# Optimization experiments

Measured on AMD Instinct MI355X. Metric: run time of the kernel, lower is better.

## Reference

```python
import jax, jax.numpy as jnp
import numpy as np

T, H = 2048, 1024
NH, NKV, HD = 8, 2, 128
E, TOPK, NG, TKG = 16, 4, 4, 2
F, FS = 1024, 1024
EPS = 1e-6
ROUTED_SCALE = 2.0
THETA = 10000.0


def _rmsnorm(x, w):
    return x * jax.lax.rsqrt(jnp.mean(x * x, axis=-1, keepdims=True) + EPS) * w


def setup_inputs() -> dict:
    key = jax.random.key(0)
    ks = jax.random.split(key, 12)
    s = 0.02
    return {
        "hidden_states": jax.random.normal(ks[0], (T, H), jnp.float32),
        "residual": jax.random.normal(ks[1], (T, H), jnp.float32),
        "position_ids": jnp.arange(T, dtype=jnp.int32),
        "ln1_w": jnp.ones((H,), jnp.float32),
        "qkv_w": s * jax.random.normal(ks[2], (H, (NH + 2 * NKV) * HD), jnp.float32),
        "qnorm_w": jnp.ones((HD,), jnp.float32),
        "knorm_w": jnp.ones((HD,), jnp.float32),
        "dense_w": s * jax.random.normal(ks[3], (NH * HD, H), jnp.float32),
        "ln2_w": jnp.ones((H,), jnp.float32),
        "gate_w": s * jax.random.normal(ks[4], (H, E), jnp.float32),
        "expert_bias": 0.1 * jax.random.normal(ks[5], (E,), jnp.float32),
        "w13": s * jax.random.normal(ks[6], (E, H, 2 * F), jnp.float32),
        "w2": s * jax.random.normal(ks[7], (E, F, H), jnp.float32),
        "ws_gate_up": s * jax.random.normal(ks[8], (H, 2 * FS), jnp.float32),
        "ws_down": s * jax.random.normal(ks[9], (FS, H), jnp.float32),
    }


def block_forward(hidden_states, residual, position_ids, ln1_w, qkv_w, qnorm_w,
                  knorm_w, dense_w, ln2_w, gate_w, expert_bias, w13, w2,
                  ws_gate_up, ws_down):
    # fused add + RMSNorm (input_layernorm with residual)
    resid = hidden_states + residual
    h = _rmsnorm(resid, ln1_w)

    # --- attention ---
    qkv = h @ qkv_w  # [T, (NH+2*NKV)*HD]
    q = qkv[:, : NH * HD].reshape(T, NH, HD)
    k = qkv[:, NH * HD : (NH + NKV) * HD].reshape(T, NKV, HD)
    v = qkv[:, (NH + NKV) * HD :].reshape(T, NKV, HD)
    q = _rmsnorm(q, qnorm_w)  # qk-norm per head_dim
    k = _rmsnorm(k, knorm_w)

    # neox-style RoPE over full head_dim
    inv_freq = 1.0 / (THETA ** (jnp.arange(0, HD, 2, dtype=jnp.float32) / HD))
    ang = position_ids.astype(jnp.float32)[:, None] * inv_freq[None, :]  # [T, HD/2]
    cos = jnp.cos(ang)[:, None, :]
    sin = jnp.sin(ang)[:, None, :]

    def rope(x):
        x1, x2 = x[..., : HD // 2], x[..., HD // 2 :]
        return jnp.concatenate([x1 * cos - x2 * sin, x2 * cos + x1 * sin], axis=-1)

    q, k = rope(q), rope(k)
    rep = NH // NKV
    kr = jnp.repeat(k, rep, axis=1)  # [T, NH, HD]
    vr = jnp.repeat(v, rep, axis=1)

    scores = jnp.einsum("qhd,khd->hqk", q, kr) * (HD ** -0.5)
    causal = jnp.tril(jnp.ones((T, T), bool))
    scores = jnp.where(causal[None], scores, jnp.finfo(scores.dtype).min)
    probs = jax.nn.softmax(scores, axis=-1)
    ctx = jnp.einsum("hqk,khd->qhd", probs, vr).reshape(T, NH * HD)
    attn_out = ctx @ dense_w

    # fused add + RMSNorm (post_attention_layernorm)
    resid2 = attn_out + resid
    h2 = _rmsnorm(resid2, ln2_w)

    # --- MoE router: sigmoid scoring + correction bias, grouped top-k ---
    logits = h2.astype(jnp.float32) @ gate_w  # router in fp32
    s_scores = jax.nn.sigmoid(logits)  # [T, E]
    sfc = s_scores + expert_bias[None, :]
    gview = sfc.reshape(T, NG, E // NG)
    gscores = jax.lax.top_k(gview, 2)[0].sum(-1)  # sum of top-2 per group
    gidx = jax.lax.top_k(gscores, TKG)[1]  # [T, TKG]
    gmask = jax.nn.one_hot(gidx, NG, dtype=sfc.dtype).sum(1)  # [T, NG]
    smask = jnp.repeat(gmask, E // NG, axis=1)  # [T, E]
    masked = jnp.where(smask > 0, sfc, -jnp.inf)
    topk_idx = jax.lax.top_k(masked, TOPK)[1]  # [T, TOPK]
    topk_w = jnp.take_along_axis(s_scores, topk_idx, axis=1)  # weights w/o bias
    topk_w = topk_w / (topk_w.sum(-1, keepdims=True) + 1e-20)  # renormalize
    combine = (jax.nn.one_hot(topk_idx, E, dtype=topk_w.dtype) * topk_w[..., None]).sum(1)  # [T, E]

    # routed experts (dense-over-experts reference for the grouped GEMM)
    gu = jnp.einsum("th,ehf->tef", h2, w13)  # [T, E, 2F]
    g, u = gu[..., :F], gu[..., F:]
    act = jax.nn.silu(g) * u
    y = jnp.einsum("tef,efh->teh", act, w2)
    routed = jnp.einsum("teh,te->th", y, combine) * ROUTED_SCALE

    # shared expert (SwiGLU MLP)
    su = h2 @ ws_gate_up
    shared = (jax.nn.silu(su[:, :FS]) * su[:, FS:]) @ ws_down

    mlp_out = routed + shared
    return mlp_out, resid2


def reference(hidden_states, residual, position_ids, ln1_w, qkv_w, qnorm_w,
              knorm_w, dense_w, ln2_w, gate_w, expert_bias, w13, w2,
              ws_gate_up, ws_down):
    return block_forward(hidden_states, residual, position_ids, ln1_w, qkv_w,
                         qnorm_w, knorm_w, dense_w, ln2_w, gate_w, expert_bias,
                         w13, w2, ws_gate_up, ws_down)
```

## Files before the change

kernel.cpp:

```cpp
#include <hip/hip_runtime.h>
#include <hip/hip_bf16.h>


#define T_TOK 2048
#define H_DIM 1024
#define NHEAD 8
#define NKVH 2
#define HDIM 128
#define QKV_DIM 1536
#define E_EXP 16
#define TOPKE 4
#define F_DIM 1024
#define FS_DIM 1024
#define NPAIR (T_TOK*TOPKE)
#define EPS_F 1e-6f

#define DEV __device__ __forceinline__

typedef __attribute__((ext_vector_type(4))) float f32x4;
typedef __attribute__((ext_vector_type(8))) short s16x8;

DEV float us2f(unsigned short u){ return __uint_as_float(((unsigned int)u)<<16); }
DEV unsigned short f2us(float f){
  __hip_bfloat16 b = __float2bfloat16(f);
  unsigned short u; __builtin_memcpy(&u,&b,2); return u;
}

DEV void gl2lds16(const void* g, void* l){
  __builtin_amdgcn_global_load_lds(
      (const __attribute__((address_space(1))) void*)g,
      (__attribute__((address_space(3))) void*)l, 16, 0, 0);
}

DEV int crow(int qt){ int a=qt>>2, b=qt&3; return (a+1)*(2*a+b); }

DEV float bred_sum(float v, float* sm){
  #pragma unroll
  for(int o=32;o>0;o>>=1) v += __shfl_down(v,o);
  int w = threadIdx.x>>6, l = threadIdx.x&63;
  __syncthreads();
  if(l==0) sm[w]=v;
  __syncthreads();
  return sm[0]+sm[1]+sm[2]+sm[3];
}

__global__ __launch_bounds__(256) void k_cvt_t(const float* __restrict__ in,
    unsigned short* __restrict__ out, int Kd, int Nd){
  const int z = blockIdx.z;
  const int kb = blockIdx.y*32, nb = blockIdx.x*32;
  __shared__ float Lt[32][33];
  const int tid = threadIdx.x;
  const int r = tid>>3, c4 = (tid&7)*4;
  const float* src = in + (long long)z*Kd*Nd + (long long)(kb+r)*Nd + nb + c4;
  float4 v = *(const float4*)src;
  Lt[r][c4+0]=v.x; Lt[r][c4+1]=v.y; Lt[r][c4+2]=v.z; Lt[r][c4+3]=v.w;
  __syncthreads();
  ushort4 o;
  o.x = f2us(Lt[c4+0][r]); o.y = f2us(Lt[c4+1][r]);
  o.z = f2us(Lt[c4+2][r]); o.w = f2us(Lt[c4+3][r]);
  *(ushort4*)(out + (long long)z*Nd*Kd + (long long)(nb+r)*Kd + kb + c4) = o;
}

__global__ __launch_bounds__(256) void k_cvt_t3(const float* __restrict__ in,
    unsigned short* __restrict__ oh, unsigned short* __restrict__ ol,
    int Kd, int Nd){
  const int kb = blockIdx.y*32, nb = blockIdx.x*32;
  __shared__ float Lt[32][33];
  const int tid = threadIdx.x;
  const int r = tid>>3, c4 = (tid&7)*4;
  const float* src = in + (long long)(kb+r)*Nd + nb + c4;
  float4 v = *(const float4*)src;
  Lt[r][c4+0]=v.x; Lt[r][c4+1]=v.y; Lt[r][c4+2]=v.z; Lt[r][c4+3]=v.w;
  __syncthreads();
  ushort4 h4, l4;
  float f;
  f = Lt[c4+0][r]; h4.x = f2us(f); l4.x = f2us(f - us2f(h4.x));
  f = Lt[c4+1][r]; h4.y = f2us(f); l4.y = f2us(f - us2f(h4.y));
  f = Lt[c4+2][r]; h4.z = f2us(f); l4.z = f2us(f - us2f(h4.z));
  f = Lt[c4+3][r]; h4.w = f2us(f); l4.w = f2us(f - us2f(h4.w));
  const long long ob = (long long)(nb+r)*Kd + kb + c4;
  *(ushort4*)(oh + ob) = h4;
  *(ushort4*)(ol + ob) = l4;
}

template<bool GROUPED, bool GATHER>
__global__ __launch_bounds__(256) void gemm_mfma(
    const unsigned short* __restrict__ A, int lda,
    const unsigned short* __restrict__ Bt, int ldbt, long long bstride,
    unsigned short* __restrict__ C, int ldc,
    const int* __restrict__ rowidx, const int* __restrict__ grpoff,
    int Mdense, int K){
  const int z = blockIdx.z;
  const int rb = GROUPED ? grpoff[z] : 0;
  const int re = GROUPED ? grpoff[z+1] : Mdense;
  const int m0 = rb + blockIdx.y*128;
  if(m0 >= re) return;
  const int n0 = blockIdx.x*128;
  const unsigned short* Bz = Bt + (long long)z*bstride;

  __shared__ unsigned short As[128][32];
  __shared__ unsigned short Bs[128][32];

  const int tid = threadIdx.x;
  const int s0 = tid, s1 = tid+256;
  int gr0 = m0 + (s0>>2), gr1 = m0 + (s1>>2);
  if(GROUPED){ gr0 = min(gr0, re-1); gr1 = min(gr1, re-1); }
  if(GATHER){ gr0 = rowidx[gr0]; gr1 = rowidx[gr1]; }
  const unsigned short* ag0 = A + (long long)gr0*lda + (s0&3)*8;
  const unsigned short* ag1 = A + (long long)gr1*lda + (s1&3)*8;
  const unsigned short* bg0 = Bz + (long long)(n0 + (s0>>2))*ldbt + (s0&3)*8;
  const unsigned short* bg1 = Bz + (long long)(n0 + (s1>>2))*ldbt + (s1&3)*8;
  char* asb = (char*)&As[0][0];
  char* bsb = (char*)&Bs[0][0];
  const int wb = (tid & 192)*16;

  const int w = tid>>6, lane = tid&63;
  const int wm = (w>>1)*64, wn = (w&1)*64;
  const int fr = lane&15, q8 = (lane>>4)*8;

  f32x4 zero = {0.f,0.f,0.f,0.f};
  f32x4 acc[4][4];
  #pragma unroll
  for(int mi=0;mi<4;mi++)
    #pragma unroll
    for(int ni=0;ni<4;ni++) acc[mi][ni]=zero;

  for(int k0=0;k0<K;k0+=32){
    __syncthreads();
    gl2lds16(ag0 + k0, asb + wb);
    gl2lds16(ag1 + k0, asb + 4096 + wb);
    gl2lds16(bg0 + k0, bsb + wb);
    gl2lds16(bg1 + k0, bsb + 4096 + wb);
    __syncthreads();
    s16x8 af[4], bf[4];
    #pragma unroll
    for(int mi=0;mi<4;mi++) af[mi] = *(const s16x8*)&As[wm+mi*16+fr][q8];
    #pragma unroll
    for(int ni=0;ni<4;ni++) bf[ni] = *(const s16x8*)&Bs[wn+ni*16+fr][q8];
    #pragma unroll
    for(int mi=0;mi<4;mi++)
      #pragma unroll
      for(int ni=0;ni<4;ni++)
        acc[mi][ni] = __builtin_amdgcn_mfma_f32_16x16x32_bf16(af[mi], bf[ni], acc[mi][ni], 0,0,0);
  }
  const int q4 = (lane>>4)*4;
  #pragma unroll
  for(int mi=0;mi<4;mi++)
    #pragma unroll
    for(int ni=0;ni<4;ni++){
      const int col = n0 + wn + ni*16 + fr;
      #pragma unroll
      for(int r=0;r<4;r++){
        const int row = m0 + wm + mi*16 + q4 + r;
        if(row < re) C[(long long)row*ldc + col] = f2us(acc[mi][ni][r]);
      }
    }
}

template<int EPI_ADD>
__global__ __launch_bounds__(256) void gemm_mfma3(
    const unsigned short* __restrict__ Ah, const unsigned short* __restrict__ Al, int lda,
    const unsigned short* __restrict__ Bh, const unsigned short* __restrict__ Bl, int ldbt,
    float* __restrict__ C, int ldc, const float* __restrict__ D, int K){
  const int m0 = blockIdx.y*128;
  const int n0 = blockIdx.x*128;

  __shared__ unsigned short Ash[128][32];
  __shared__ unsigned short Asl[128][32];
  __shared__ unsigned short Bsh[128][32];
  __shared__ unsigned short Bsl[128][32];

  const int tid = threadIdx.x;
  const int s0 = tid, s1 = tid+256;
  const long long ar0 = (long long)(m0 + (s0>>2))*lda + (s0&3)*8;
  const long long ar1 = (long long)(m0 + (s1>>2))*lda + (s1&3)*8;
  const long long br0 = (long long)(n0 + (s0>>2))*ldbt + (s0&3)*8;
  const long long br1 = (long long)(n0 + (s1>>2))*ldbt + (s1&3)*8;
  char* ahb = (char*)&Ash[0][0];
  char* alb = (char*)&Asl[0][0];
  char* bhb = (char*)&Bsh[0][0];
  char* blb = (char*)&Bsl[0][0];
  const int wb = (tid & 192)*16;

  const int w = tid>>6, lane = tid&63;
  const int wm = (w>>1)*64, wn = (w&1)*64;
  const int fr = lane&15, q8 = (lane>>4)*8;

  f32x4 zero = {0.f,0.f,0.f,0.f};
  f32x4 acc[4][4];
  #pragma unroll
  for(int mi=0;mi<4;mi++)
    #pragma unroll
    for(int ni=0;ni<4;ni++) acc[mi][ni]=zero;

  for(int k0=0;k0<K;k0+=32){
    __syncthreads();
    gl2lds16(Ah + ar0 + k0, ahb + wb);
    gl2lds16(Ah + ar1 + k0, ahb + 4096 + wb);
    gl2lds16(Al + ar0 + k0, alb + wb);
    gl2lds16(Al + ar1 + k0, alb + 4096 + wb);
    gl2lds16(Bh + br0 + k0, bhb + wb);
    gl2lds16(Bh + br1 + k0, bhb + 4096 + wb);
    gl2lds16(Bl + br0 + k0, blb + wb);
    gl2lds16(Bl + br1 + k0, blb + 4096 + wb);
    __syncthreads();
    s16x8 afh[4], afl[4], bfh[4], bfl[4];
    #pragma unroll
    for(int mi=0;mi<4;mi++){
      afh[mi] = *(const s16x8*)&Ash[wm+mi*16+fr][q8];
      afl[mi] = *(const s16x8*)&Asl[wm+mi*16+fr][q8];
    }
    #pragma unroll
    for(int ni=0;ni<4;ni++){
      bfh[ni] = *(const s16x8*)&Bsh[wn+ni*16+fr][q8];
      bfl[ni] = *(const s16x8*)&Bsl[wn+ni*16+fr][q8];
    }
    #pragma unroll
    for(int mi=0;mi<4;mi++)
      #pragma unroll
      for(int ni=0;ni<4;ni++){
        acc[mi][ni] = __builtin_amdgcn_mfma_f32_16x16x32_bf16(afh[mi], bfh[ni], acc[mi][ni], 0,0,0);
        acc[mi][ni] = __builtin_amdgcn_mfma_f32_16x16x32_bf16(afh[mi], bfl[ni], acc[mi][ni], 0,0,0);
        acc[mi][ni] = __builtin_amdgcn_mfma_f32_16x16x32_bf16(afl[mi], bfh[ni], acc[mi][ni], 0,0,0);
      }
  }
  const int q4 = (lane>>4)*4;
  #pragma unroll
  for(int mi=0;mi<4;mi++)
    #pragma unroll
    for(int ni=0;ni<4;ni++){
      const int col = n0 + wn + ni*16 + fr;
      #pragma unroll
      for(int r=0;r<4;r++){
        const int row = m0 + wm + mi*16 + q4 + r;
        float v = acc[mi][ni][r];
        if(EPI_ADD) v += D[(long long)row*ldc + col];
        C[(long long)row*ldc + col] = v;
      }
    }
}

__global__ __launch_bounds__(256) void k_silu(const unsigned short* __restrict__ gu,
    unsigned short* __restrict__ act){
  const int r = blockIdx.x, c = threadIdx.x*4;
  const ushort4 g4 = *(const ushort4*)(gu + (long long)r*2048 + c);
  const ushort4 u4 = *(const ushort4*)(gu + (long long)r*2048 + 1024 + c);
  float g[4] = {us2f(g4.x),us2f(g4.y),us2f(g4.z),us2f(g4.w)};
  float u[4] = {us2f(u4.x),us2f(u4.y),us2f(u4.z),us2f(u4.w)};
  ushort4 o;
  o.x = f2us((g[0]/(1.f+__expf(-g[0])))*u[0]);
  o.y = f2us((g[1]/(1.f+__expf(-g[1])))*u[1]);
  o.z = f2us((g[2]/(1.f+__expf(-g[2])))*u[2]);
  o.w = f2us((g[3]/(1.f+__expf(-g[3])))*u[3]);
  *(ushort4*)(act + (long long)r*1024 + c) = o;
}

__global__ __launch_bounds__(256) void k_add_rmsnorm(const float* __restrict__ hs,
    const float* __restrict__ rs, const float* __restrict__ w,
    float* __restrict__ resid, unsigned short* __restrict__ ah,
    unsigned short* __restrict__ al){
  int t = blockIdx.x, tid = threadIdx.x;
  __shared__ float sm[4];
  const long base = (long)t*H_DIM;
  float x[4]; float ss = 0.f;
  #pragma unroll
  for(int i=0;i<4;i++){
    int c = tid + i*256;
    float v = hs[base+c] + rs[base+c];
    x[i]=v; resid[base+c]=v; ss += v*v;
  }
  float tot = bred_sum(ss, sm);
  float rms = rsqrtf(tot/(float)H_DIM + EPS_F);
  #pragma unroll
  for(int i=0;i<4;i++){
    int c = tid + i*256;
    float v = x[i]*rms*w[c];
    unsigned short hh = f2us(v);
    ah[base+c] = hh;
    al[base+c] = f2us(v - us2f(hh));
  }
}

__global__ __launch_bounds__(64) void k_qkv_post(const float* __restrict__ qkv,
    const float* __restrict__ qw, const float* __restrict__ kw,
    const int* __restrict__ pos,
    float* __restrict__ qb, float* __restrict__ kb, float* __restrict__ vb){
  int slot = blockIdx.x, t = blockIdx.y, lane = threadIdx.x;
  const float* x = qkv + (long long)t*QKV_DIM + slot*HDIM;
  float x0 = x[lane], x1 = x[lane+64];
  if(slot < 10){
    float ss = x0*x0 + x1*x1;
    #pragma unroll
    for(int o=32;o>0;o>>=1) ss += __shfl_xor(ss,o);
    float rms = rsqrtf(ss/(float)HDIM + EPS_F);
    const float* w = (slot<8)? qw : kw;
    float n0 = x0*rms*w[lane];
    float n1 = x1*rms*w[lane+64];
    float p = (float)pos[t];
    float invf = __expf(-((float)lane/64.f)*9.210340371976184f);
    float ang = p*invf;
    float s = sinf(ang), c = cosf(ang);
    float o0 = n0*c - n1*s;
    float o1 = n1*c + n0*s;
    float* dst = (slot<8)? (qb + ((long long)slot*T_TOK + t)*HDIM)
                         : (kb + ((long long)(slot-8)*T_TOK + t)*HDIM);
    dst[lane]=o0; dst[lane+64]=o1;
  } else {
    float* dst = vb + ((long long)(slot-10)*T_TOK + t)*HDIM;
    dst[lane]=x0; dst[lane+64]=x1;
  }
}

#define FBQ 32
#define FBK 128
__global__ __launch_bounds__(256,2) void k_flash(const float* __restrict__ qb,
    const float* __restrict__ kb, const float* __restrict__ vb,
    float* __restrict__ ctx, float* __restrict__ Op1, float* __restrict__ Op2,
    float* __restrict__ Ml){
  const int b = blockIdx.x;
  const int u0 = (17*b)>>1, u1 = (17*(b+1))>>1;
  const int tid = threadIdx.x;
  const int lane = tid & 63;
  const int w = tid >> 6;
  const int tx = tid & 31;
  const int ty = tid >> 5;
  const int fsw = tx & 7;

  __shared__ float4 smem4[4096];
  char*  smem = (char*)smem4;
  float* Ksf  = (float*)smem;
  float* Psf  = (float*)(smem + 49152);

  const float scale = 0.08838834764831845f;

  int h = u0/544;
  int r = u0 - h*544;
  int qt = 0;
  while(qt < 63 && crow(qt+1) <= r) qt++;
  int kt = r - crow(qt);

  int u = u0;
  while(u < u1){
    const int nkt = (qt>>2) + 1;
    const int q0 = qt * FBQ;
    const int kv = h >> 2;
    const float* kbase = kb + (long long)kv*T_TOK*HDIM;
    const float* vbase = vb + (long long)kv*T_TOK*HDIM;
    const float* qrow0 = qb + ((long long)h*T_TOK + q0 + ty*4)*HDIM;
    const int segN = min(nkt - kt, u1 - u);
    const int ktEnd = kt + segN;

    float m_[4], l_[4], O[4][4];
    #pragma unroll
    for(int qi=0;qi<4;qi++){
      m_[qi] = -1e30f; l_[qi] = 0.f;
      #pragma unroll
      for(int j=0;j<4;j++) O[qi][j] = 0.f;
    }

    for(; kt<ktEnd; kt++){
      const int k0 = kt * FBK;
      __syncthreads();
      {
        const float* kcur = kbase + (long long)k0*HDIM;
        #pragma unroll
        for(int i=0;i<16;i++){
          const int rbase = (w<<5) + (i<<1);
          const int f = (i>>1) & 7;
          const float* src = kcur + (long long)(rbase + (lane>>5))*HDIM
                                  + (((lane&31)^f)<<2);
          gl2lds16(src, smem + rbase*512);
        }
      }
      __syncthreads();

      float s[4][4];
      #pragma unroll
      for(int qi=0;qi<4;qi++)
        #pragma unroll
        for(int ki=0;ki<4;ki++) s[qi][ki] = 0.f;

      #pragma unroll 2
      for(int dc=0; dc<32; dc++){
        float4 qv[4];
        #pragma unroll
        for(int qi=0;qi<4;qi++) qv[qi] = *(const float4*)(qrow0 + qi*HDIM + dc*4);
        float4 kf[4];
        #pragma unroll
        for(int ki=0;ki<4;ki++)
          kf[ki] = *(const float4*)&Ksf[(size_t)(4*tx+ki)*128 + ((dc ^ fsw)<<2)];
        #pragma unroll
        for(int qi=0;qi<4;qi++)
          #pragma unroll
          for(int ki=0;ki<4;ki++){
            s[qi][ki] = fmaf(qv[qi].x, kf[ki].x, s[qi][ki]);
            s[qi][ki] = fmaf(qv[qi].y, kf[ki].y, s[qi][ki]);
            s[qi][ki] = fmaf(qv[qi].z, kf[ki].z, s[qi][ki]);
            s[qi][ki] = fmaf(qv[qi].w, kf[ki].w, s[qi][ki]);
          }
      }

      const bool last = (kt == nkt-1);
      float rm[4];
      #pragma unroll
      for(int qi=0;qi<4;qi++){
        #pragma unroll
        for(int ki=0;ki<4;ki++){
          float v = s[qi][ki]*scale;
          if(last && (k0 + 4*tx + ki > q0 + ty*4 + qi)) v = -1e30f;
          s[qi][ki] = v;
        }
        rm[qi] = fmaxf(fmaxf(s[qi][0],s[qi][1]), fmaxf(s[qi][2],s[qi][3]));
      }
      #pragma unroll
      for(int o=1;o<32;o<<=1){
        #pragma unroll
        for(int qi=0;qi<4;qi++) rm[qi] = fmaxf(rm[qi], __shfl_xor(rm[qi], o));
      }
      float a_[4], rs[4];
      #pragma unroll
      for(int qi=0;qi<4;qi++){
        float mn = fmaxf(m_[qi], rm[qi]);
        a_[qi] = __expf(m_[qi] - mn);
        m_[qi] = mn;
        float rr = 0.f;
        #pragma unroll
        for(int ki=0;ki<4;ki++){ s[qi][ki] = __expf(s[qi][ki] - mn); rr += s[qi][ki]; }
        rs[qi] = rr;
      }
      #pragma unroll
      for(int o=1;o<32;o<<=1){
        #pragma unroll
        for(int qi=0;qi<4;qi++) rs[qi] += __shfl_xor(rs[qi], o);
      }
      #pragma unroll
      for(int qi=0;qi<4;qi++){
        l_[qi] = l_[qi]*a_[qi] + rs[qi];
        #pragma unroll
        for(int j=0;j<4;j++) O[qi][j] *= a_[qi];
      }

      __syncthreads();
      #pragma unroll
      for(int ki=0;ki<4;ki++){
        float4 pv;
        pv.x = s[0][ki]; pv.y = s[1][ki]; pv.z = s[2][ki]; pv.w = s[3][ki];
        *(float4*)&Psf[(size_t)(4*tx+ki)*32 + ((ty ^ fsw)<<2)] = pv;
      }
      __syncthreads();

      const float* vcur = vbase + (long long)k0*HDIM + tx*4;
      #pragma unroll 4
      for(int k=0;k<FBK;k++){
        float4 p4 = *(const float4*)&Psf[(size_t)k*32 + ((ty ^ ((k>>2)&7))<<2)];
        float4 vv = *(const float4*)(vcur + (size_t)k*HDIM);
        O[0][0]=fmaf(p4.x,vv.x,O[0][0]); O[0][1]=fmaf(p4.x,vv.y,O[0][1]);
        O[0][2]=fmaf(p4.x,vv.z,O[0][2]); O[0][3]=fmaf(p4.x,vv.w,O[0][3]);
        O[1][0]=fmaf(p4.y,vv.x,O[1][0]); O[1][1]=fmaf(p4.y,vv.y,O[1][1]);
        O[1][2]=fmaf(p4.y,vv.z,O[1][2]); O[1][3]=fmaf(p4.y,vv.w,O[1][3]);
        O[2][0]=fmaf(p4.z,vv.x,O[2][0]); O[2][1]=fmaf(p4.z,vv.y,O[2][1]);
        O[2][2]=fmaf(p4.z,vv.z,O[2][2]); O[2][3]=fmaf(p4.z,vv.w,O[2][3]);
        O[3][0]=fmaf(p4.w,vv.x,O[3][0]); O[3][1]=fmaf(p4.w,vv.y,O[3][1]);
        O[3][2]=fmaf(p4.w,vv.z,O[3][2]); O[3][3]=fmaf(p4.w,vv.w,O[3][3]);
      }
    }

    {
      const int R = (h<<6) + qt;
      const int S = h*544 + crow(qt);
      const int bS = (2*S+1)/17;
      const int j = b - bS;
      #pragma unroll
      for(int qi=0;qi<4;qi++){
        const int row = ty*4 + qi;
        float4 o4 = make_float4(O[qi][0],O[qi][1],O[qi][2],O[qi][3]);
        if(j==0){
          *(float4*)(ctx + (long long)(q0+row)*(NHEAD*HDIM) + h*HDIM + tx*4) = o4;
        } else if(j==1){
          *(float4*)(Op1 + (long long)R*4096 + row*128 + tx*4) = o4;
        } else {
          *(float4*)(Op2 + (long long)R*4096 + row*128 + tx*4) = o4;
        }
        if(tx==0){
          Ml[((R*3+j)<<6) + row*2 + 0] = m_[qi];
          Ml[((R*3+j)<<6) + row*2 + 1] = l_[qi];
        }
      }
    }

    u += segN;
    if(ktEnd == nkt){ kt = 0; qt++; if(qt == 64){ qt = 0; h++; } }
    else kt = ktEnd;
  }
}

__global__ __launch_bounds__(256) void k_fmerge(const float* __restrict__ ctx,
    const float* __restrict__ Op1, const float* __restrict__ Op2,
    const float* __restrict__ Ml, unsigned short* __restrict__ ch,
    unsigned short* __restrict__ cl){
  const int wv = threadIdx.x>>6, lane = threadIdx.x&63;
  const int gr = blockIdx.x*4 + wv;
  const int R = gr>>5, q = gr&31;
  const int h = R>>6, qt = R&63;
  const int nkt = (qt>>2)+1;
  const int S = h*544 + crow(qt);
  const int bS = (2*S+1)/17;
  const int bE = (2*(S+nkt-1)+1)/17;
  const int parts = bE - bS + 1;
  const float* src0 = ctx + (long long)(qt*32+q)*(NHEAD*HDIM) + h*HDIM + lane*2;
  float2 o0 = *(const float2*)src0;
  const float* mlb = Ml + ((R*3)<<6) + q*2;
  const float m0 = mlb[0], l0 = mlb[1];
  float ox, oy;
  if(parts == 1){
    float inv = 1.f/l0;
    ox = o0.x*inv; oy = o0.y*inv;
  } else {
    const float m1 = mlb[64], l1 = mlb[65];
    float2 o1 = *(const float2*)(Op1 + (long long)R*4096 + q*128 + lane*2);
    if(parts == 2){
      float mx = fmaxf(m0,m1);
      float a0 = __expf(m0-mx), a1 = __expf(m1-mx);
      float inv = 1.f/(l0*a0 + l1*a1);
      ox = (o0.x*a0 + o1.x*a1)*inv;
      oy = (o0.y*a0 + o1.y*a1)*inv;
    } else {
      const float m2 = mlb[128], l2 = mlb[129];
      float2 o2 = *(const float2*)(Op2 + (long long)R*4096 + q*128 + lane*2);
      float mx = fmaxf(fmaxf(m0,m1),m2);
      float a0 = __expf(m0-mx), a1 = __expf(m1-mx), a2 = __expf(m2-mx);
      float inv = 1.f/(l0*a0 + l1*a1 + l2*a2);
      ox = (o0.x*a0 + o1.x*a1 + o2.x*a2)*inv;
      oy = (o0.y*a0 + o1.y*a1 + o2.y*a2)*inv;
    }
  }
  const long long idx = (long long)(qt*32+q)*(NHEAD*HDIM) + h*HDIM + lane*2;
  unsigned short hx = f2us(ox), hy = f2us(oy);
  ch[idx] = hx;   cl[idx] = f2us(ox - us2f(hx));
  ch[idx+1] = hy; cl[idx+1] = f2us(oy - us2f(hy));
}

__global__ __launch_bounds__(256) void k_rms2(const float* __restrict__ r2,
    const float* __restrict__ w, float* __restrict__ h2f,
    unsigned short* __restrict__ h2b){
  int t = blockIdx.x, tid = threadIdx.x;
  __shared__ float sm[4];
  const long base = (long)t*H_DIM;
  float x[4]; float ss=0.f;
  #pragma unroll
  for(int i=0;i<4;i++){
    int c = tid+i*256;
    float v = r2[base+c];
    x[i]=v; ss += v*v;
  }
  float tot = bred_sum(ss, sm);
  float rms = rsqrtf(tot/(float)H_DIM + EPS_F);
  #pragma unroll
  for(int i=0;i<4;i++){
    int c = tid+i*256;
    float v = x[i]*rms*w[c];
    h2f[base+c] = v;
    h2b[base+c] = f2us(v);
  }
}

__global__ __launch_bounds__(256) void k_router(const float* __restrict__ h2,
    const float* __restrict__ gw, const float* __restrict__ eb,
    int* __restrict__ topk_idx, float* __restrict__ topk_w, int* __restrict__ counts){
  int t = blockIdx.x, tid = threadIdx.x;
  int e = tid & 15, seg = tid >> 4;
  const float* hrow = h2 + (long long)t*H_DIM;
  float part = 0.f;
  #pragma unroll 4
  for(int i=0;i<64;i++){
    int hh = seg*64 + i;
    part += hrow[hh]*gw[hh*E_EXP + e];
  }
  __shared__ float pm[16][17];
  __shared__ float sS[16], sfc[16];
  pm[seg][e] = part;
  __syncthreads();
  if(tid < 16){
    float l = 0.f;
    #pragma unroll
    for(int s=0;s<16;s++) l += pm[s][tid];
    float sg = 1.f/(1.f+expf(-l));
    sS[tid]=sg; sfc[tid]=sg+eb[tid];
  }
  __syncthreads();
  if(tid==0){
    float gs[4];
    #pragma unroll
    for(int g=0; g<4; g++){
      float m1=-1e30f, m2=-1e30f;
      for(int j=0;j<4;j++){
        float v=sfc[g*4+j];
        if(v>m1){ m2=m1; m1=v; } else if(v>m2){ m2=v; }
      }
      gs[g]=m1+m2;
    }
    int g1=0; for(int g=1;g<4;g++) if(gs[g]>gs[g1]) g1=g;
    int g2=-1; for(int g=0;g<4;g++){ if(g==g1) continue; if(g2<0||gs[g]>gs[g2]) g2=g; }
    bool taken[16];
    #pragma unroll
    for(int i=0;i<16;i++) taken[i]=false;
    int idx[4];
    for(int j=0;j<4;j++){
      int best=-1; float bv=-1e30f;
      for(int i=0;i<16;i++){
        int g=i>>2;
        if(g!=g1 && g!=g2) continue;
        if(taken[i]) continue;
        if(best<0 || sfc[i]>bv){ best=i; bv=sfc[i]; }
      }
      taken[best]=true; idx[j]=best;
    }
    float w[4]; float s=0.f;
    #pragma unroll
    for(int j=0;j<4;j++){ w[j]=sS[idx[j]]; s+=w[j]; }
    s += 1e-20f;
    #pragma unroll
    for(int j=0;j<4;j++){
      topk_idx[t*4+j]=idx[j];
      topk_w[t*4+j]=w[j]/s;
      atomicAdd(&counts[idx[j]],1);
    }
  }
}

__global__ void k_zero(int* __restrict__ counts){ if(threadIdx.x<16) counts[threadIdx.x]=0; }

__global__ void k_scan(const int* __restrict__ counts, int* __restrict__ offs, int* __restrict__ cursor){
  if(threadIdx.x==0){
    int s=0;
    for(int e2=0;e2<16;e2++){ offs[e2]=s; cursor[e2]=s; s+=counts[e2]; }
    offs[16]=s;
  }
}

__global__ __launch_bounds__(256) void k_scatter(const int* __restrict__ topk_idx,
    int* __restrict__ cursor, int* __restrict__ pair_tok, int* __restrict__ tok2pair){
  int i = blockIdx.x*256 + threadIdx.x;
  int e = topk_idx[i];
  int pos = atomicAdd(&cursor[e],1);
  pair_tok[pos] = i>>2;
  tok2pair[i] = pos;
}

__global__ __launch_bounds__(256) void k_combine(const unsigned short* __restrict__ y,
    const unsigned short* __restrict__ sout, const int* __restrict__ tok2pair,
    const float* __restrict__ topk_w, float* __restrict__ out0){
  int t = blockIdx.x, tid = threadIdx.x;
  int p[4]; float w[4];
  #pragma unroll
  for(int j=0;j<4;j++){ p[j]=tok2pair[t*4+j]; w[j]=topk_w[t*4+j]*2.0f; }
  const long base = (long)t*H_DIM;
  #pragma unroll
  for(int i=0;i<4;i++){
    int c = tid + i*256;
    float v = us2f(sout[base+c]);
    #pragma unroll
    for(int j=0;j<4;j++) v += w[j]*us2f(y[(long long)p[j]*H_DIM + c]);
    out0[base+c] = v;
  }
}

extern "C" void kernel_launch(void* const* d_in, const int* in_sizes, int n_in,
                              void* d_out, int out_size, void* d_ws, size_t ws_size,
                              hipStream_t stream) {
  const float* hs   = (const float*)d_in[0];
  const float* rsd  = (const float*)d_in[1];
  const int*   pos  = (const int*)d_in[2];
  const float* ln1  = (const float*)d_in[3];
  const float* qkvw = (const float*)d_in[4];
  const float* qnw  = (const float*)d_in[5];
  const float* knw  = (const float*)d_in[6];
  const float* dw   = (const float*)d_in[7];
  const float* ln2  = (const float*)d_in[8];
  const float* gw   = (const float*)d_in[9];
  const float* eb   = (const float*)d_in[10];
  const float* w13  = (const float*)d_in[11];
  const float* w2   = (const float*)d_in[12];
  const float* wsgu = (const float*)d_in[13];
  const float* wsd  = (const float*)d_in[14];
  float* out0 = (float*)d_out;
  float* out1 = out0 + (size_t)T_TOK*H_DIM;

  char* W = (char*)d_ws;
  float* resid = (float*)(W + 0);
  unsigned short* ah = (unsigned short*)(W + 8388608);
  unsigned short* al = (unsigned short*)(W + 12582912);
  float* ctx   = (float*)(W + 8388608);
  float* qkv   = (float*)(W + 16777216);
  float* qb    = (float*)(W + 29360128);
  float* h2f   = (float*)(W + 37748736);
  float* kb    = (float*)(W + 46137344);
  float* vb    = (float*)(W + 48234496);
  float* Op1   = (float*)(W + 16777216);
  float* Ml    = (float*)(W + 25165824);
  float* Op2   = (float*)(W + 37748736);
  unsigned short* cth = (unsigned short*)(W + 29360128);
  unsigned short* ctl = (unsigned short*)(W + 33554432);
  unsigned short* qwt_h = (unsigned short*)(W + 37748736);
  unsigned short* qwt_l = (unsigned short*)(W + 40894464);
  unsigned short* dwt_h = (unsigned short*)(W + 50331648);
  unsigned short* dwt_l = (unsigned short*)(W + 52428800);
  unsigned short* gu    = (unsigned short*)(W + 8388608);
  unsigned short* ybuf  = (unsigned short*)(W + 8388608);
  unsigned short* sgu   = (unsigned short*)(W + 16777216);
  unsigned short* sact  = (unsigned short*)(W + 0);
  unsigned short* sout  = (unsigned short*)(W + 46137344);
  unsigned short* h2b   = (unsigned short*)(W + 50331648);
  unsigned short* act   = (unsigned short*)(W + 54525952);
  unsigned short* w13t  = (unsigned short*)(W + 71303168);
  unsigned short* w2t   = (unsigned short*)(W + 138412032);
  unsigned short* wsgut = (unsigned short*)(W + 171966464);
  unsigned short* wsdt  = (unsigned short*)(W + 176160768);
  float* topkw = (float*)(W + 178257920);
  int* topki   = (int*)(W + 178290688);
  int* ptok    = (int*)(W + 178323456);
  int* t2p     = (int*)(W + 178356224);
  int* cnt     = (int*)(W + 178388992);
  int* offs    = (int*)(W + 178389056);
  int* cur     = (int*)(W + 178389184);

  k_cvt_t<<<dim3(64,32,16), 256, 0, stream>>>(w13,  w13t,  1024, 2048);
  k_cvt_t<<<dim3(32,32,16), 256, 0, stream>>>(w2,   w2t,   1024, 1024);
  k_cvt_t<<<dim3(64,32,1),  256, 0, stream>>>(wsgu, wsgut, 1024, 2048);
  k_cvt_t<<<dim3(32,32,1),  256, 0, stream>>>(wsd,  wsdt,  1024, 1024);
  k_cvt_t3<<<dim3(48,32,1), 256, 0, stream>>>(qkvw, qwt_h, qwt_l, 1024, 1536);
  k_cvt_t3<<<dim3(32,32,1), 256, 0, stream>>>(dw,   dwt_h, dwt_l, 1024, 1024);
  k_add_rmsnorm<<<T_TOK, 256, 0, stream>>>(hs, rsd, ln1, resid, ah, al);
  gemm_mfma3<0><<<dim3(QKV_DIM/128, T_TOK/128), 256, 0, stream>>>(
      ah, al, 1024, qwt_h, qwt_l, 1024, qkv, QKV_DIM, nullptr, 1024);
  k_qkv_post<<<dim3(12, T_TOK), 64, 0, stream>>>(qkv, qnw, knw, pos, qb, kb, vb);
  k_flash<<<512, 256, 0, stream>>>(qb, kb, vb, ctx, Op1, Op2, Ml);
  k_fmerge<<<4096, 256, 0, stream>>>(ctx, Op1, Op2, Ml, cth, ctl);
  gemm_mfma3<1><<<dim3(H_DIM/128, T_TOK/128), 256, 0, stream>>>(
      cth, ctl, 1024, dwt_h, dwt_l, 1024, out1, H_DIM, resid, 1024);
  k_rms2<<<T_TOK, 256, 0, stream>>>(out1, ln2, h2f, h2b);
  k_zero<<<1, 64, 0, stream>>>(cnt);
  k_router<<<T_TOK, 256, 0, stream>>>(h2f, gw, eb, topki, topkw, cnt);
  k_scan<<<1, 64, 0, stream>>>(cnt, offs, cur);
  k_scatter<<<NPAIR/256, 256, 0, stream>>>(topki, cur, ptok, t2p);
  gemm_mfma<false,false><<<dim3(16,16,1), 256, 0, stream>>>(
      h2b, 1024, wsgut, 1024, 0, sgu, 2048, nullptr, nullptr, T_TOK, 1024);
  k_silu<<<T_TOK, 256, 0, stream>>>(sgu, sact);
  gemm_mfma<false,false><<<dim3(8,16,1), 256, 0, stream>>>(
      sact, 1024, wsdt, 1024, 0, sout, 1024, nullptr, nullptr, T_TOK, 1024);
  gemm_mfma<true,true><<<dim3(16,64,16), 256, 0, stream>>>(
      h2b, 1024, w13t, 1024, (long long)2048*1024, gu, 2048, ptok, offs, 0, 1024);
  k_silu<<<NPAIR, 256, 0, stream>>>(gu, act);
  gemm_mfma<true,false><<<dim3(8,64,16), 256, 0, stream>>>(
      act, 1024, w2t, 1024, (long long)1024*1024, ybuf, 1024, nullptr, offs, 0, 1024);
  k_combine<<<T_TOK, 256, 0, stream>>>(ybuf, sout, t2p, topkw, out0);
}
```

Baseline: 935.8 us.

## Compute flash attention QK^T with split-bf16 MFMA and rebalance work over 768 blocks

```diff
diff --git a/kernel.cpp b/kernel.cpp
--- a/kernel.cpp
+++ b/kernel.cpp
@@ -284,7 +284,9 @@
 __global__ __launch_bounds__(64) void k_qkv_post(const float* __restrict__ qkv,
     const float* __restrict__ qw, const float* __restrict__ kw,
     const int* __restrict__ pos,
-    float* __restrict__ qb, float* __restrict__ kb, float* __restrict__ vb){
+    unsigned short* __restrict__ qbh, unsigned short* __restrict__ qbl,
+    unsigned short* __restrict__ kbh, unsigned short* __restrict__ kbl,
+    float* __restrict__ vb){
   int slot = blockIdx.x, t = blockIdx.y, lane = threadIdx.x;
   const float* x = qkv + (long long)t*QKV_DIM + slot*HDIM;
   float x0 = x[lane], x1 = x[lane+64];
@@ -302,9 +304,14 @@
     float s = sinf(ang), c = cosf(ang);
     float o0 = n0*c - n1*s;
     float o1 = n1*c + n0*s;
-    float* dst = (slot<8)? (qb + ((long long)slot*T_TOK + t)*HDIM)
-                         : (kb + ((long long)(slot-8)*T_TOK + t)*HDIM);
-    dst[lane]=o0; dst[lane+64]=o1;
+    long long base = (slot<8)? ((long long)slot*T_TOK + t)*HDIM
+                             : ((long long)(slot-8)*T_TOK + t)*HDIM;
+    unsigned short* dh = (slot<8)? qbh : kbh;
+    unsigned short* dl = (slot<8)? qbl : kbl;
+    unsigned short h0 = f2us(o0);
+    dh[base+lane] = h0;        dl[base+lane] = f2us(o0 - us2f(h0));
+    unsigned short h1 = f2us(o1);
+    dh[base+lane+64] = h1;     dl[base+lane+64] = f2us(o1 - us2f(h1));
   } else {
     float* dst = vb + ((long long)(slot-10)*T_TOK + t)*HDIM;
     dst[lane]=x0; dst[lane+64]=x1;
@@ -313,40 +320,46 @@
 
 #define FBQ 32
 #define FBK 128
-__global__ __launch_bounds__(256,2) void k_flash(const float* __restrict__ qb,
-    const float* __restrict__ kb, const float* __restrict__ vb,
-    float* __restrict__ ctx, float* __restrict__ Op1, float* __restrict__ Op2,
+__global__ __launch_bounds__(256,3) void k_flash(
+    const unsigned short* __restrict__ qbh, const unsigned short* __restrict__ qbl,
+    const unsigned short* __restrict__ kbh, const unsigned short* __restrict__ kbl,
+    const float* __restrict__ vb, float* __restrict__ ctx,
+    float* __restrict__ Op1, float* __restrict__ Op2, float* __restrict__ Op3,
     float* __restrict__ Ml){
   const int b = blockIdx.x;
-  const int u0 = (17*b)>>1, u1 = (17*(b+1))>>1;
+  const int u0 = (17*b)/3, u1 = (17*(b+1))/3;
   const int tid = threadIdx.x;
   const int lane = tid & 63;
   const int w = tid >> 6;
   const int tx = tid & 31;
   const int ty = tid >> 5;
-  const int fsw = tx & 7;
-
-  __shared__ float4 smem4[4096];
-  char*  smem = (char*)smem4;
-  float* Ksf  = (float*)smem;
-  float* Psf  = (float*)(smem + 49152);
+  const int fr = lane & 15;
+  const int l4 = lane >> 4;
+
+  __shared__ float4 ps4[1024];
+  __shared__ float Ms[4][32];
+  __shared__ float Ls[4][32];
+  __shared__ float Mn[32];
+  float* Psf = (float*)ps4;
 
   const float scale = 0.08838834764831845f;
 
   int h = u0/544;
-  int r = u0 - h*544;
+  int r0 = u0 - h*544;
   int qt = 0;
-  while(qt < 63 && crow(qt+1) <= r) qt++;
-  int kt = r - crow(qt);
+  while(qt < 63 && crow(qt+1) <= r0) qt++;
+  int kt = r0 - crow(qt);
 
   int u = u0;
   while(u < u1){
     const int nkt = (qt>>2) + 1;
     const int q0 = qt * FBQ;
     const int kv = h >> 2;
-    const float* kbase = kb + (long long)kv*T_TOK*HDIM;
+    const unsigned short* qhp = qbh + ((long long)h*T_TOK + q0)*HDIM;
+    const unsigned short* qlp = qbl + ((long long)h*T_TOK + q0)*HDIM;
+    const unsigned short* khb = kbh + (long long)kv*T_TOK*HDIM;
+    const unsigned short* klb = kbl + (long long)kv*T_TOK*HDIM;
     const float* vbase = vb + (long long)kv*T_TOK*HDIM;
-    const float* qrow0 = qb + ((long long)h*T_TOK + q0 + ty*4)*HDIM;
     const int segN = min(nkt - kt, u1 - u);
     const int ktEnd = kt + segN;
 
@@ -360,95 +373,132 @@
 
     for(; kt<ktEnd; kt++){
       const int k0 = kt * FBK;
+      f32x4 sa[2][2];
+      f32x4 zero = {0.f,0.f,0.f,0.f};
+      sa[0][0]=zero; sa[0][1]=zero; sa[1][0]=zero; sa[1][1]=zero;
+      const unsigned short* khp = khb + (long long)(k0 + w*32)*HDIM;
+      const unsigned short* klp = klb + (long long)(k0 + w*32)*HDIM;
+      #pragma unroll
+      for(int dw=0; dw<4; dw++){
+        const int doff = dw*32 + l4*8;
+        s16x8 a0h = *(const s16x8*)(qhp + (long long)fr*HDIM + doff);
+        s16x8 a0l = *(const s16x8*)(qlp + (long long)fr*HDIM + doff);
+        s16x8 a1h = *(const s16x8*)(qhp + (long long)(16+fr)*HDIM + doff);
+        s16x8 a1l = *(const s16x8*)(qlp + (long long)(16+fr)*HDIM + doff);
+        s16x8 b0h = *(const s16x8*)(khp + (long long)fr*HDIM + doff);
+        s16x8 b0l = *(const s16x8*)(klp + (long long)fr*HDIM + doff);
+        s16x8 b1h = *(const s16x8*)(khp + (long long)(16+fr)*HDIM + doff);
+        s16x8 b1l = *(const s16x8*)(klp + (long long)(16+fr)*HDIM + doff);
+        sa[0][0] = __builtin_amdgcn_mfma_f32_16x16x32_bf16(a0h,b0h,sa[0][0],0,0,0);
+        sa[0][0] = __builtin_amdgcn_mfma_f32_16x16x32_bf16(a0h,b0l,sa[0][0],0,0,0);
+        sa[0][0] = __builtin_amdgcn_mfma_f32_16x16x32_bf16(a0l,b0h,sa[0][0],0,0,0);
+        sa[0][1] = __builtin_amdgcn_mfma_f32_16x16x32_bf16(a0h,b1h,sa[0][1],0,0,0);
+        sa[0][1] = __builtin_amdgcn_mfma_f32_16x16x32_bf16(a0h,b1l,sa[0][1],0,0,0);
+        sa[0][1] = __builtin_amdgcn_mfma_f32_16x16x32_bf16(a0l,b1h,sa[0][1],0,0,0);
+        sa[1][0] = __builtin_amdgcn_mfma_f32_16x16x32_bf16(a1h,b0h,sa[1][0],0,0,0);
+        sa[1][0] = __builtin_amdgcn_mfma_f32_16x16x32_bf16(a1h,b0l,sa[1][0],0,0,0);
+        sa[1][0] = __builtin_amdgcn_mfma_f32_16x16x32_bf16(a1l,b0h,sa[1][0],0,0,0);
+        sa[1][1] = __builtin_amdgcn_mfma_f32_16x16x32_bf16(a1h,b1h,sa[1][1],0,0,0);
+        sa[1][1] = __builtin_amdgcn_mfma_f32_16x16x32_bf16(a1h,b1l,sa[1][1],0,0,0);
+        sa[1][1] = __builtin_amdgcn_mfma_f32_16x16x32_bf16(a1l,b1h,sa[1][1],0,0,0);
+      }
+
+      const bool last = (kt == nkt-1);
+      const int kg0 = k0 + w*32 + fr;
+      const int kg1 = kg0 + 16;
+      float rm[2][4];
+      #pragma unroll
+      for(int q2=0;q2<2;q2++){
+        #pragma unroll
+        for(int r=0;r<4;r++){
+          const int qg = q0 + q2*16 + l4*4 + r;
+          float v0 = sa[q2][0][r]*scale;
+          float v1 = sa[q2][1][r]*scale;
+          if(last && kg0 > qg) v0 = -1e30f;
+          if(last && kg1 > qg) v1 = -1e30f;
+          sa[q2][0][r] = v0; sa[q2][1][r] = v1;
+          rm[q2][r] = fmaxf(v0, v1);
+        }
+      }
+      #pragma unroll
+      for(int o=1;o<16;o<<=1){
+        #pragma unroll
+        for(int q2=0;q2<2;q2++)
+          #pragma unroll
+          for(int r=0;r<4;r++)
+            rm[q2][r] = fmaxf(rm[q2][r], __shfl_xor(rm[q2][r], o));
+      }
+      if(fr==0){
+        #pragma unroll
+        for(int q2=0;q2<2;q2++)
+          #pragma unroll
+          for(int r=0;r<4;r++)
+            Ms[w][q2*16 + l4*4 + r] = rm[q2][r];
+      }
       __syncthreads();
-      {
-        const float* kcur = kbase + (long long)k0*HDIM;
-        #pragma unroll
-        for(int i=0;i<16;i++){
-          const int rbase = (w<<5) + (i<<1);
-          const int f = (i>>1) & 7;
-          const float* src = kcur + (long long)(rbase + (lane>>5))*HDIM
-                                  + (((lane&31)^f)<<2);
-          gl2lds16(src, smem + rbase*512);
+
+      #pragma unroll
+      for(int qi=0;qi<4;qi++){
+        const int row = ty*4 + qi;
+        float g = fmaxf(fmaxf(Ms[0][row],Ms[1][row]), fmaxf(Ms[2][row],Ms[3][row]));
+        float mn = fmaxf(m_[qi], g);
+        float a = __expf(m_[qi] - mn);
+        m_[qi] = mn;
+        l_[qi] *= a;
+        #pragma unroll
+        for(int j=0;j<4;j++) O[qi][j] *= a;
+      }
+      if(tx==0){
+        #pragma unroll
+        for(int qi=0;qi<4;qi++) Mn[ty*4+qi] = m_[qi];
+      }
+      __syncthreads();
+
+      float rsum[2][4];
+      #pragma unroll
+      for(int q2=0;q2<2;q2++)
+        #pragma unroll
+        for(int r=0;r<4;r++) rsum[q2][r] = 0.f;
+      #pragma unroll
+      for(int q2=0;q2<2;q2++){
+        float mnv[4];
+        #pragma unroll
+        for(int r=0;r<4;r++) mnv[r] = Mn[q2*16 + l4*4 + r];
+        #pragma unroll
+        for(int k2=0;k2<2;k2++){
+          const int kl = w*32 + k2*16 + fr;
+          const int qc = q2*4 + l4;
+          float4 pv;
+          float p;
+          p = __expf(sa[q2][k2][0] - mnv[0]); pv.x = p; rsum[q2][0] += p;
+          p = __expf(sa[q2][k2][1] - mnv[1]); pv.y = p; rsum[q2][1] += p;
+          p = __expf(sa[q2][k2][2] - mnv[2]); pv.z = p; rsum[q2][2] += p;
+          p = __expf(sa[q2][k2][3] - mnv[3]); pv.w = p; rsum[q2][3] += p;
+          *(float4*)&Psf[(size_t)kl*32 + ((qc ^ ((kl>>2)&7))<<2)] = pv;
         }
       }
+      #pragma unroll
+      for(int o=1;o<16;o<<=1){
+        #pragma unroll
+        for(int q2=0;q2<2;q2++)
+          #pragma unroll
+          for(int r=0;r<4;r++)
+            rsum[q2][r] += __shfl_xor(rsum[q2][r], o);
+      }
+      if(fr==0){
+        #pragma unroll
+        for(int q2=0;q2<2;q2++)
+          #pragma unroll
+          for(int r=0;r<4;r++)
+            Ls[w][q2*16 + l4*4 + r] = rsum[q2][r];
+      }
       __syncthreads();
 
-      float s[4][4];
-      #pragma unroll
-      for(int qi=0;qi<4;qi++)
-        #pragma unroll
-        for(int ki=0;ki<4;ki++) s[qi][ki] = 0.f;
-
-      #pragma unroll 2
-      for(int dc=0; dc<32; dc++){
-        float4 qv[4];
-        #pragma unroll
-        for(int qi=0;qi<4;qi++) qv[qi] = *(const float4*)(qrow0 + qi*HDIM + dc*4);
-        float4 kf[4];
-        #pragma unroll
-        for(int ki=0;ki<4;ki++)
-          kf[ki] = *(const float4*)&Ksf[(size_t)(4*tx+ki)*128 + ((dc ^ fsw)<<2)];
-        #pragma unroll
-        for(int qi=0;qi<4;qi++)
-          #pragma unroll
-          for(int ki=0;ki<4;ki++){
-            s[qi][ki] = fmaf(qv[qi].x, kf[ki].x, s[qi][ki]);
-            s[qi][ki] = fmaf(qv[qi].y, kf[ki].y, s[qi][ki]);
-            s[qi][ki] = fmaf(qv[qi].z, kf[ki].z, s[qi][ki]);
-            s[qi][ki] = fmaf(qv[qi].w, kf[ki].w, s[qi][ki]);
-          }
-      }
-
-      const bool last = (kt == nkt-1);
-      float rm[4];
       #pragma unroll
       for(int qi=0;qi<4;qi++){
-        #pragma unroll
-        for(int ki=0;ki<4;ki++){
-          float v = s[qi][ki]*scale;
-          if(last && (k0 + 4*tx + ki > q0 + ty*4 + qi)) v = -1e30f;
-          s[qi][ki] = v;
-        }
-        rm[qi] = fmaxf(fmaxf(s[qi][0],s[qi][1]), fmaxf(s[qi][2],s[qi][3]));
-      }
-      #pragma unroll
-      for(int o=1;o<32;o<<=1){
-        #pragma unroll
-        for(int qi=0;qi<4;qi++) rm[qi] = fmaxf(rm[qi], __shfl_xor(rm[qi], o));
-      }
-      float a_[4], rs[4];
-      #pragma unroll
-      for(int qi=0;qi<4;qi++){
-        float mn = fmaxf(m_[qi], rm[qi]);
-        a_[qi] = __expf(m_[qi] - mn);
-        m_[qi] = mn;
-        float rr = 0.f;
-        #pragma unroll
-        for(int ki=0;ki<4;ki++){ s[qi][ki] = __expf(s[qi][ki] - mn); rr += s[qi][ki]; }
-        rs[qi] = rr;
-      }
-      #pragma unroll
-      for(int o=1;o<32;o<<=1){
-        #pragma unroll
-        for(int qi=0;qi<4;qi++) rs[qi] += __shfl_xor(rs[qi], o);
-      }
-      #pragma unroll
-      for(int qi=0;qi<4;qi++){
-        l_[qi] = l_[qi]*a_[qi] + rs[qi];
-        #pragma unroll
-        for(int j=0;j<4;j++) O[qi][j] *= a_[qi];
-      }
-
-      __syncthreads();
-      #pragma unroll
-      for(int ki=0;ki<4;ki++){
-        float4 pv;
-        pv.x = s[0][ki]; pv.y = s[1][ki]; pv.z = s[2][ki]; pv.w = s[3][ki];
-        *(float4*)&Psf[(size_t)(4*tx+ki)*32 + ((ty ^ fsw)<<2)] = pv;
-      }
-      __syncthreads();
-
+        const int row = ty*4 + qi;
+        l_[qi] += Ls[0][row] + Ls[1][row] + Ls[2][row] + Ls[3][row];
+      }
       const float* vcur = vbase + (long long)k0*HDIM + tx*4;
       #pragma unroll 4
       for(int k=0;k<FBK;k++){
@@ -468,7 +518,7 @@
     {
       const int R = (h<<6) + qt;
       const int S = h*544 + crow(qt);
-      const int bS = (2*S+1)/17;
+      const int bS = (3*S+2)/17;
       const int j = b - bS;
       #pragma unroll
       for(int qi=0;qi<4;qi++){
@@ -478,12 +528,14 @@
           *(float4*)(ctx + (long long)(q0+row)*(NHEAD*HDIM) + h*HDIM + tx*4) = o4;
         } else if(j==1){
           *(float4*)(Op1 + (long long)R*4096 + row*128 + tx*4) = o4;
+        } else if(j==2){
+          *(float4*)(Op2 + (long long)R*4096 + row*128 + tx*4) = o4;
         } else {
-          *(float4*)(Op2 + (long long)R*4096 + row*128 + tx*4) = o4;
+          *(float4*)(Op3 + (long long)R*4096 + row*128 + tx*4) = o4;
         }
         if(tx==0){
-          Ml[((R*3+j)<<6) + row*2 + 0] = m_[qi];
-          Ml[((R*3+j)<<6) + row*2 + 1] = l_[qi];
+          Ml[((R*4+j)<<6) + row*2 + 0] = m_[qi];
+          Ml[((R*4+j)<<6) + row*2 + 1] = l_[qi];
         }
       }
     }
@@ -496,48 +548,40 @@
 
 __global__ __launch_bounds__(256) void k_fmerge(const float* __restrict__ ctx,
     const float* __restrict__ Op1, const float* __restrict__ Op2,
-    const float* __restrict__ Ml, unsigned short* __restrict__ ch,
-    unsigned short* __restrict__ cl){
-  const int wv = threadIdx.x>>6, lane = threadIdx.x&63;
+    const float* __restrict__ Op3, const float* __restrict__ Ml,
+    unsigned short* __restrict__ ch, unsigned short* __restrict__ cl){
+  const int wv = threadIdx.x>>6, ln = threadIdx.x&63;
   const int gr = blockIdx.x*4 + wv;
   const int R = gr>>5, q = gr&31;
   const int h = R>>6, qt = R&63;
   const int nkt = (qt>>2)+1;
   const int S = h*544 + crow(qt);
-  const int bS = (2*S+1)/17;
-  const int bE = (2*(S+nkt-1)+1)/17;
+  const int bS = (3*S+2)/17;
+  const int bE = (3*(S+nkt-1)+2)/17;
   const int parts = bE - bS + 1;
-  const float* src0 = ctx + (long long)(qt*32+q)*(NHEAD*HDIM) + h*HDIM + lane*2;
-  float2 o0 = *(const float2*)src0;
-  const float* mlb = Ml + ((R*3)<<6) + q*2;
-  const float m0 = mlb[0], l0 = mlb[1];
-  float ox, oy;
-  if(parts == 1){
-    float inv = 1.f/l0;
-    ox = o0.x*inv; oy = o0.y*inv;
-  } else {
-    const float m1 = mlb[64], l1 = mlb[65];
-    float2 o1 = *(const float2*)(Op1 + (long long)R*4096 + q*128 + lane*2);
-    if(parts == 2){
-      float mx = fmaxf(m0,m1);
-      float a0 = __expf(m0-mx), a1 = __expf(m1-mx);
-      float inv = 1.f/(l0*a0 + l1*a1);
-      ox = (o0.x*a0 + o1.x*a1)*inv;
-      oy = (o0.y*a0 + o1.y*a1)*inv;
-    } else {
-      const float m2 = mlb[128], l2 = mlb[129];
-      float2 o2 = *(const float2*)(Op2 + (long long)R*4096 + q*128 + lane*2);
-      float mx = fmaxf(fmaxf(m0,m1),m2);
-      float a0 = __expf(m0-mx), a1 = __expf(m1-mx), a2 = __expf(m2-mx);
-      float inv = 1.f/(l0*a0 + l1*a1 + l2*a2);
-      ox = (o0.x*a0 + o1.x*a1 + o2.x*a2)*inv;
-      oy = (o0.y*a0 + o1.y*a1 + o2.y*a2)*inv;
-    }
-  }
-  const long long idx = (long long)(qt*32+q)*(NHEAD*HDIM) + h*HDIM + lane*2;
+  const long long cix = (long long)(qt*32+q)*(NHEAD*HDIM) + h*HDIM + ln*2;
+  float2 o0 = *(const float2*)(ctx + cix);
+  const float* mlb = Ml + ((R*4)<<6) + q*2;
+  float m0 = mlb[0],  l0v = mlb[1];
+  float2 o1 = make_float2(0.f,0.f), o2 = o1, o3 = o1;
+  float m1=-1e30f,l1v=0.f,m2=-1e30f,l2v=0.f,m3=-1e30f,l3v=0.f;
+  float mx = m0;
+  if(parts>1){ m1=mlb[64];  l1v=mlb[65];
+    o1 = *(const float2*)(Op1 + (long long)R*4096 + q*128 + ln*2); mx=fmaxf(mx,m1); }
+  if(parts>2){ m2=mlb[128]; l2v=mlb[129];
+    o2 = *(const float2*)(Op2 + (long long)R*4096 + q*128 + ln*2); mx=fmaxf(mx,m2); }
+  if(parts>3){ m3=mlb[192]; l3v=mlb[193];
+    o3 = *(const float2*)(Op3 + (long long)R*4096 + q*128 + ln*2); mx=fmaxf(mx,m3); }
+  float a0 = __expf(m0-mx);
+  float a1 = (parts>1)? __expf(m1-mx) : 0.f;
+  float a2 = (parts>2)? __expf(m2-mx) : 0.f;
+  float a3 = (parts>3)? __expf(m3-mx) : 0.f;
+  float inv = 1.f/(l0v*a0 + l1v*a1 + l2v*a2 + l3v*a3);
+  float ox = (o0.x*a0 + o1.x*a1 + o2.x*a2 + o3.x*a3)*inv;
+  float oy = (o0.y*a0 + o1.y*a1 + o2.y*a2 + o3.y*a3)*inv;
   unsigned short hx = f2us(ox), hy = f2us(oy);
-  ch[idx] = hx;   cl[idx] = f2us(ox - us2f(hx));
-  ch[idx+1] = hy; cl[idx+1] = f2us(oy - us2f(hy));
+  ch[cix]   = hx; cl[cix]   = f2us(ox - us2f(hx));
+  ch[cix+1] = hy; cl[cix+1] = f2us(oy - us2f(hy));
 }
 
 __global__ __launch_bounds__(256) void k_rms2(const float* __restrict__ r2,
@@ -692,13 +736,16 @@
   unsigned short* al = (unsigned short*)(W + 12582912);
   float* ctx   = (float*)(W + 8388608);
   float* qkv   = (float*)(W + 16777216);
-  float* qb    = (float*)(W + 29360128);
   float* h2f   = (float*)(W + 37748736);
-  float* kb    = (float*)(W + 46137344);
   float* vb    = (float*)(W + 48234496);
+  unsigned short* qbh = (unsigned short*)(W + 29360128);
+  unsigned short* qbl = (unsigned short*)(W + 33554432);
+  unsigned short* kbh = (unsigned short*)(W + 46137344);
+  unsigned short* kbl = (unsigned short*)(W + 47185920);
   float* Op1   = (float*)(W + 16777216);
   float* Ml    = (float*)(W + 25165824);
   float* Op2   = (float*)(W + 37748736);
+  float* Op3   = (float*)(W + 54525952);
   unsigned short* cth = (unsigned short*)(W + 29360128);
   unsigned short* ctl = (unsigned short*)(W + 33554432);
   unsigned short* qwt_h = (unsigned short*)(W + 37748736);
@@ -733,9 +780,10 @@
   k_add_rmsnorm<<<T_TOK, 256, 0, stream>>>(hs, rsd, ln1, resid, ah, al);
   gemm_mfma3<0><<<dim3(QKV_DIM/128, T_TOK/128), 256, 0, stream>>>(
       ah, al, 1024, qwt_h, qwt_l, 1024, qkv, QKV_DIM, nullptr, 1024);
-  k_qkv_post<<<dim3(12, T_TOK), 64, 0, stream>>>(qkv, qnw, knw, pos, qb, kb, vb);
-  k_flash<<<512, 256, 0, stream>>>(qb, kb, vb, ctx, Op1, Op2, Ml);
-  k_fmerge<<<4096, 256, 0, stream>>>(ctx, Op1, Op2, Ml, cth, ctl);
+  k_qkv_post<<<dim3(12, T_TOK), 64, 0, stream>>>(qkv, qnw, knw, pos,
+      qbh, qbl, kbh, kbl, vb);
+  k_flash<<<768, 256, 0, stream>>>(qbh, qbl, kbh, kbl, vb, ctx, Op1, Op2, Op3, Ml);
+  k_fmerge<<<4096, 256, 0, stream>>>(ctx, Op1, Op2, Op3, Ml, cth, ctl);
   gemm_mfma3<1><<<dim3(H_DIM/128, T_TOK/128), 256, 0, stream>>>(
       cth, ctl, 1024, dwt_h, dwt_l, 1024, out1, H_DIM, resid, 1024);
   k_rms2<<<T_TOK, 256, 0, stream>>>(out1, ln2, h2f, h2b);
```

Result: slower. 1.000 ms (+6.9%).
